# Kernel tuning notes

Hardware: AMD Instinct MI355X
Metric: run time of the kernel (lower is better)

Reference implementation:

```python
import jax, jax.numpy as jnp
import numpy as np

N_HEADS = 16
ROPE_BASE = 10000.0


def apply_rope(x):
    # x: [B, H, T, D]; rotate interleaved pairs along last dim, positions along T
    B, H, T, D = x.shape
    half = D // 2
    inv_freq = 1.0 / (ROPE_BASE ** (jnp.arange(0, half, dtype=jnp.float32) * 2.0 / D))
    angles = jnp.arange(T, dtype=jnp.float32)[:, None] * inv_freq[None, :]  # [T, half]
    cos = jnp.cos(angles).astype(x.dtype)  # [T, half]
    sin = jnp.sin(angles).astype(x.dtype)
    xp = x.reshape(B, H, T, half, 2)
    x1, x2 = xp[..., 0], xp[..., 1]
    out = jnp.stack([x1 * cos - x2 * sin, x1 * sin + x2 * cos], axis=-1)
    return out.reshape(B, H, T, D)


def setup_inputs() -> dict:
    key = jax.random.key(0)
    k1, k2, k3 = jax.random.split(key, 3)
    C = 1024
    x = jax.random.normal(k1, (2, 2048, C), dtype=jnp.float32)
    w_qkv = jax.random.normal(k2, (C, 3 * C), dtype=jnp.float32) * (1.0 / np.sqrt(C))
    w_out = jax.random.normal(k3, (C, C), dtype=jnp.float32) * (1.0 / np.sqrt(C))
    return {"x": x, "w_qkv": w_qkv, "w_out": w_out}


def reference(x, w_qkv, w_out):
    B, T, C = x.shape
    H = N_HEADS
    D = C // H
    qkv = (x @ w_qkv).reshape(B, T, 3, H, D)
    q, k, v = qkv[:, :, 0], qkv[:, :, 1], qkv[:, :, 2]  # [B, T, H, D]
    q = jnp.transpose(q, (0, 2, 1, 3))  # [B, H, T, D]
    k = jnp.transpose(k, (0, 2, 1, 3))
    v = jnp.transpose(v, (0, 2, 1, 3))
    q = apply_rope(q)
    k = apply_rope(k)
    scale = 1.0 / np.sqrt(D)
    scores = jnp.einsum('bhqd,bhkd->bhqk', q, k) * scale
    causal = jnp.tril(jnp.ones((T, T), dtype=bool))
    scores = jnp.where(causal, scores, jnp.finfo(scores.dtype).min)
    attn = jax.nn.softmax(scores, axis=-1)
    out = jnp.einsum('bhqk,bhkd->bhqd', attn, v)  # [B, H, T, D]
    out = jnp.transpose(out, (0, 2, 1, 3)).reshape(B, T, C)
    return out @ w_out
```

## Files before the change

kernel.cpp:

```cpp
#include <hip/hip_runtime.h>
#include <hip/hip_bf16.h>

typedef __attribute__((ext_vector_type(8))) short v8s;
typedef __attribute__((ext_vector_type(4))) float v4f;
typedef __attribute__((ext_vector_type(16))) float v16f;

typedef const __attribute__((address_space(1))) void* gas_ptr;
typedef __attribute__((address_space(3))) void* las_ptr;

#define MFMA16(a, b, c) __builtin_amdgcn_mfma_f32_16x16x32_bf16((a), (b), (c), 0, 0, 0)
#define MFMA32(a, b, c) __builtin_amdgcn_mfma_f32_32x32x16_bf16((a), (b), (c), 0, 0, 0)

__device__ __forceinline__ void gload_lds16(const void* g, void* l) {
  __builtin_amdgcn_global_load_lds((gas_ptr)g, (las_ptr)l, 16, 0, 0);
}

__device__ __forceinline__ unsigned short f2bf(float f) {
  unsigned int u = __float_as_uint(f);
  u += 0x7FFFu + ((u >> 16) & 1u);
  return (unsigned short)(u >> 16);
}
__device__ __forceinline__ float bf2f(unsigned short h) {
  return __uint_as_float(((unsigned int)h) << 16);
}

__device__ __forceinline__ unsigned cvt_pk_bf16(float lo, float hi) {
  unsigned r;
  asm("v_cvt_pk_bf16_f32 %0, %1, %2" : "=v"(r) : "v"(lo), "v"(hi));
  return r;
}

__global__ __launch_bounds__(256) void k_convert(const float* __restrict__ in,
                                                 unsigned short* __restrict__ out, int n4) {
  int i = blockIdx.x * 256 + threadIdx.x;
  if (i >= n4) return;
  float4 v = ((const float4*)in)[i];
  ushort4 o;
  o.x = f2bf(v.x); o.y = f2bf(v.y); o.z = f2bf(v.z); o.w = f2bf(v.w);
  ((ushort4*)out)[i] = o;
}

__global__ __launch_bounds__(256) void k_transpose_convert(const float* __restrict__ in,
                                                           unsigned short* __restrict__ out,
                                                           int R, int C) {
  __shared__ __attribute__((aligned(16))) unsigned short tb[64 * 72];
  const int r0 = blockIdx.y * 64, c0 = blockIdx.x * 64;
  const int tid = threadIdx.x;
#pragma unroll
  for (int j = 0; j < 4; ++j) {
    int slot = tid + 256 * j;
    int row = slot >> 4, q4 = (slot & 15) * 4;
    float4 v = *(const float4*)&in[(size_t)(r0 + row) * C + c0 + q4];
    ushort4 o;
    o.x = f2bf(v.x); o.y = f2bf(v.y); o.z = f2bf(v.z); o.w = f2bf(v.w);
    *(ushort4*)&tb[row * 72 + q4] = o;
  }
  __syncthreads();
#pragma unroll
  for (int j = 0; j < 4; ++j) {
    int slot = tid + 256 * j;
    int crow = slot >> 4, t4 = (slot & 15) * 4;
    ushort4 o;
    o.x = tb[(t4 + 0) * 72 + crow];
    o.y = tb[(t4 + 1) * 72 + crow];
    o.z = tb[(t4 + 2) * 72 + crow];
    o.w = tb[(t4 + 3) * 72 + crow];
    *(ushort4*)&out[(size_t)(c0 + crow) * R + r0 + t4] = o;
  }
}

template <bool F32OUT>
__global__ __launch_bounds__(256) void k_gemm(const unsigned short* __restrict__ A,
                                              const unsigned short* __restrict__ Bt,
                                              void* __restrict__ Cout,
                                              int M, int N, int K) {
  __shared__ __attribute__((aligned(16))) unsigned short As[128 * 32];
  __shared__ __attribute__((aligned(16))) unsigned short Bs[128 * 32];
  const int tid = threadIdx.x;
  const int w = tid >> 6, l = tid & 63, g = l >> 4, c = l & 15;
  const int wr = w >> 1, wc = w & 1;
  const int mt = blockIdx.y * 128, nt = blockIdx.x * 128;
  const int rowc = l >> 2, kslot = (l & 3) * 8;

  v4f acc[4][4];
#pragma unroll
  for (int m = 0; m < 4; ++m)
#pragma unroll
    for (int n = 0; n < 4; ++n) acc[m][n] = (v4f){0.f, 0.f, 0.f, 0.f};

  for (int kt = 0; kt < K; kt += 32) {
    __syncthreads();
#pragma unroll
    for (int i = 0; i < 2; ++i) {
      int ch = w + 4 * i;
      gload_lds16(&A[(size_t)(mt + ch * 16 + rowc) * K + kt + kslot], &As[ch * 512]);
      gload_lds16(&Bt[(size_t)(nt + ch * 16 + rowc) * K + kt + kslot], &Bs[ch * 512]);
    }
    __syncthreads();
    v8s af[4], bfr[4];
#pragma unroll
    for (int m = 0; m < 4; ++m)
      af[m] = *(const v8s*)&As[(wr * 64 + m * 16 + c) * 32 + g * 8];
#pragma unroll
    for (int n = 0; n < 4; ++n)
      bfr[n] = *(const v8s*)&Bs[(wc * 64 + n * 16 + c) * 32 + g * 8];
#pragma unroll
    for (int m = 0; m < 4; ++m)
#pragma unroll
      for (int n = 0; n < 4; ++n)
        acc[m][n] = MFMA16(af[m], bfr[n], acc[m][n]);
  }

#pragma unroll
  for (int m = 0; m < 4; ++m)
#pragma unroll
    for (int n = 0; n < 4; ++n)
#pragma unroll
      for (int r = 0; r < 4; ++r) {
        int row = mt + wr * 64 + m * 16 + g * 4 + r;
        int col = nt + wc * 64 + n * 16 + c;
        if (F32OUT)
          ((float*)Cout)[(size_t)row * N + col] = acc[m][n][r];
        else
          ((unsigned short*)Cout)[(size_t)row * N + col] = f2bf(acc[m][n][r]);
      }
}

__global__ __launch_bounds__(256) void k_post(const unsigned short* __restrict__ qkv,
                                              unsigned short* __restrict__ qp,
                                              unsigned short* __restrict__ kp,
                                              unsigned short* __restrict__ vp) {
  __shared__ float2 cs[64 * 32];
  __shared__ __attribute__((aligned(16))) unsigned short vt[64 * 72];
  const int bh = blockIdx.y;
  const int b = bh >> 4, hd = bh & 15;
  const int t0 = blockIdx.x * 64;
  const int tid = threadIdx.x;

#pragma unroll
  for (int e = 0; e < 8; ++e) {
    int idx = tid + 256 * e;
    int tl = idx >> 5, i = idx & 31;
    float invf = exp2f(-(float)i * 0.41524101186092034f);
    float ang = (float)(t0 + tl) * invf;
    float s, cc;
    sincosf(ang, &s, &cc);
    cs[idx] = make_float2(cc, s);
  }
#pragma unroll
  for (int j = 0; j < 2; ++j) {
    int slot = tid + 256 * j;
    int row = slot >> 3, c8 = (slot & 7) * 8;
    v8s vv = *(const v8s*)&qkv[(size_t)(b * 2048 + t0 + row) * 3072 + 2048 + hd * 64 + c8];
    *(v8s*)&vt[row * 72 + c8] = vv;
  }
  __syncthreads();

#pragma unroll
  for (int j = 0; j < 2; ++j) {
    int slot = tid + 256 * j;
    int row = slot >> 3, d0 = (slot & 7) * 8;
    int t = t0 + row;
    size_t base = (size_t)(b * 2048 + t) * 3072 + hd * 64;
    const int tile = t >> 5, c32 = t & 31, kd = d0 >> 4, hh = (d0 >> 3) & 1;
    const size_t pidx = (size_t)bh * 131072 + (tile * 4 + kd) * 512 + (hh * 32 + c32) * 8;
#pragma unroll
    for (int which = 0; which < 2; ++which) {
      const float qsc = which ? 1.0f : 0.18033688011112042f;
      v8s vq = *(const v8s*)&qkv[base + which * 1024 + d0];
      union { unsigned short s[8]; v8s v; } uo;
#pragma unroll
      for (int p = 0; p < 4; ++p) {
        float2 sc = cs[row * 32 + d0 / 2 + p];
        float x1 = bf2f((unsigned short)vq[2 * p]);
        float x2 = bf2f((unsigned short)vq[2 * p + 1]);
        uo.s[2 * p]     = f2bf((x1 * sc.x - x2 * sc.y) * qsc);
        uo.s[2 * p + 1] = f2bf((x1 * sc.y + x2 * sc.x) * qsc);
      }
      unsigned short* dst = which ? kp : qp;
      *(v8s*)&dst[pidx] = uo.v;
    }
  }

#pragma unroll
  for (int jj = 0; jj < 2; ++jj) {
    int idx = tid + 256 * jj;
    int tl = idx >> 8, kc = (idx >> 7) & 1, md = (idx >> 6) & 1;
    int lp = idx & 63, hh = lp >> 5, c32 = lp & 31;
    int d = md * 32 + c32;
    int brow = tl * 32 + kc * 16 + hh * 4;
    union { unsigned short s[8]; v8s v; } uo;
#pragma unroll
    for (int jh = 0; jh < 2; ++jh)
#pragma unroll
      for (int e = 0; e < 4; ++e)
        uo.s[jh * 4 + e] = vt[(brow + jh * 8 + e) * 72 + d];
    int tileG = (t0 >> 5) + tl;
    *(v8s*)&vp[(size_t)bh * 131072 + ((tileG * 2 + kc) * 2 + md) * 512 + lp * 8] = uo.v;
  }
}

__global__ __launch_bounds__(64) void k_attn(const unsigned short* __restrict__ qp,
                                             const unsigned short* __restrict__ kp,
                                             const unsigned short* __restrict__ vp,
                                             unsigned short* __restrict__ ao,
                                             char* __restrict__ part) {
  const int bid = (int)blockIdx.x;
  const int xcd = bid & 7, s2 = bid >> 3;
  const int bh = xcd + 8 * (s2 / 160);
  const int idx = 159 - (s2 % 160);
  int j, s;
  if (idx >= 96)      { j = 48 + ((idx - 96) >> 2); s = (idx - 96) & 3; }
  else if (idx >= 48) { j = 32 + (idx - 48) / 3;    s = (idx - 48) % 3; }
  else if (idx >= 16) { j = 16 + ((idx - 16) >> 1); s = (idx - 16) & 1; }
  else                { j = idx;                    s = 0; }
  const int t0 = s * 16;
  const int t1 = (t0 + 16 < j + 1) ? (t0 + 16) : (j + 1);

  const int l = threadIdx.x;
  const int c32 = l & 31, hh = l >> 5;
  const unsigned short* Qb = qp + (size_t)bh * 131072 + j * 4 * 512;
  const unsigned short* Kb = kp + (size_t)bh * 131072;
  const unsigned short* Vb = vp + (size_t)bh * 131072;

  v8s bq[4];
#pragma unroll
  for (int kd = 0; kd < 4; ++kd) bq[kd] = *(const v8s*)&Qb[kd * 512 + l * 8];

  v16f ot0 = {0,0,0,0,0,0,0,0,0,0,0,0,0,0,0,0};
  v16f ot1 = {0,0,0,0,0,0,0,0,0,0,0,0,0,0,0,0};
  float m2 = -1e30f, lsl = 0.f;

  v8s ak[4], av0[2][2], av1[2][2];
#pragma unroll
  for (int kd = 0; kd < 4; ++kd) ak[kd] = *(const v8s*)&Kb[(t0 * 4 + kd) * 512 + l * 8];
#pragma unroll
  for (int kc = 0; kc < 2; ++kc)
#pragma unroll
    for (int md = 0; md < 2; ++md)
      av0[kc][md] = *(const v8s*)&Vb[((t0 * 2 + kc) * 2 + md) * 512 + l * 8];

  auto TILE = [&](int t, v8s (&avc)[2][2], v8s (&avn)[2][2]) {
    v16f st = {0,0,0,0,0,0,0,0,0,0,0,0,0,0,0,0};
    __builtin_amdgcn_s_setprio(1);
#pragma unroll
    for (int kd = 0; kd < 4; ++kd) st = MFMA32(ak[kd], bq[kd], st);
    __builtin_amdgcn_s_setprio(0);

    if (t + 1 < t1) {
#pragma unroll
      for (int kd = 0; kd < 4; ++kd)
        ak[kd] = *(const v8s*)&Kb[((t + 1) * 4 + kd) * 512 + l * 8];
#pragma unroll
      for (int kc = 0; kc < 2; ++kc)
#pragma unroll
        for (int md = 0; md < 2; ++md)
          avn[kc][md] = *(const v8s*)&Vb[(((t + 1) * 2 + kc) * 2 + md) * 512 + l * 8];
    }

    if (t == j) {
#pragma unroll
      for (int r = 0; r < 16; ++r) {
        int rloc = (r & 3) + 8 * (r >> 2) + 4 * hh;
        st[r] = (rloc <= c32) ? st[r] : -1e30f;
      }
    }

    float a0 = fmaxf(st[0], st[1]),   a1 = fmaxf(st[2], st[3]);
    float a2 = fmaxf(st[4], st[5]),   a3 = fmaxf(st[6], st[7]);
    float a4 = fmaxf(st[8], st[9]),   a5 = fmaxf(st[10], st[11]);
    float a6 = fmaxf(st[12], st[13]), a7 = fmaxf(st[14], st[15]);
    float b0m = fmaxf(fmaxf(a0, a1), fmaxf(a2, a3));
    float b1m = fmaxf(fmaxf(a4, a5), fmaxf(a6, a7));
    float pm = fmaxf(b0m, b1m);
    if (!__all(pm <= m2 + 8.f)) {
      float pmw = fmaxf(pm, __shfl_xor(pm, 32));
      float mn = fmaxf(m2, pmw);
      float al = exp2f(m2 - mn);
      m2 = mn;
      lsl *= al;
      ot0 *= al;
      ot1 *= al;
    }

#pragma unroll
    for (int r = 0; r < 16; ++r) st[r] = exp2f(st[r] - m2);
    float e0 = st[0] + st[1],   e1 = st[2] + st[3];
    float e2 = st[4] + st[5],   e3 = st[6] + st[7];
    float e4 = st[8] + st[9],   e5 = st[10] + st[11];
    float e6 = st[12] + st[13], e7 = st[14] + st[15];
    float f0 = e0 + e1, f1 = e2 + e3, f2 = e4 + e5, f3 = e6 + e7;
    lsl += (f0 + f1) + (f2 + f3);

    unsigned wd[8];
#pragma unroll
    for (int i = 0; i < 8; ++i) wd[i] = cvt_pk_bf16(st[2 * i], st[2 * i + 1]);
    union { unsigned u[4]; v8s v; } pb0, pb1;
    pb0.u[0] = wd[0]; pb0.u[1] = wd[1]; pb0.u[2] = wd[2]; pb0.u[3] = wd[3];
    pb1.u[0] = wd[4]; pb1.u[1] = wd[5]; pb1.u[2] = wd[6]; pb1.u[3] = wd[7];

    __builtin_amdgcn_s_setprio(1);
    ot0 = MFMA32(avc[0][0], pb0.v, ot0);
    ot1 = MFMA32(avc[0][1], pb0.v, ot1);
    ot0 = MFMA32(avc[1][0], pb1.v, ot0);
    ot1 = MFMA32(avc[1][1], pb1.v, ot1);
    __builtin_amdgcn_s_setprio(0);
  };

  int t = t0;
  for (; t + 1 < t1; t += 2) {
    TILE(t,     av0, av1);
    TILE(t + 1, av1, av0);
  }
  if (t < t1) TILE(t, av0, av1);

  const float ls = lsl + __shfl_xor(lsl, 32);
  const float inv = 1.f / ls;
  if (j < 16) {
    const int b = bh >> 4, hd = bh & 15;
    const int tq = j * 32 + c32;
    unsigned short* aop = ao + (size_t)(b * 2048 + tq) * 1024 + hd * 64;
#pragma unroll
    for (int md = 0; md < 2; ++md)
#pragma unroll
      for (int q = 0; q < 4; ++q) {
        const v16f& o = md ? ot1 : ot0;
        unsigned w0 = cvt_pk_bf16(o[4 * q + 0] * inv, o[4 * q + 1] * inv);
        unsigned w1 = cvt_pk_bf16(o[4 * q + 2] * inv, o[4 * q + 3] * inv);
        int d = md * 32 + 8 * q + 4 * hh;
        *(uint2*)&aop[d] = make_uint2(w0, w1);
      }
  } else {
    char* slot = part + ((size_t)bh * 160 + idx) * 4352;
#pragma unroll
    for (int md = 0; md < 2; ++md)
#pragma unroll
      for (int i = 0; i < 8; ++i) {
        const v16f& o = md ? ot1 : ot0;
        union { _Float16 h[2]; unsigned u; } pk;
        pk.h[0] = (_Float16)(o[2 * i] * inv);
        pk.h[1] = (_Float16)(o[2 * i + 1] * inv);
        *(unsigned*)(slot + ((md * 8 + i) * 64 + l) * 4) = pk.u;
      }
    if (hh == 0) {
      *(float*)(slot + 4096 + c32 * 4) = m2;
      *(float*)(slot + 4224 + c32 * 4) = ls;
    }
  }
}

__global__ __launch_bounds__(64) void k_comb(const char* __restrict__ part,
                                             unsigned short* __restrict__ ao) {
  const int bh = blockIdx.y;
  const int j = 16 + (int)blockIdx.x;
  const int g = j >> 4;
  const int nch = g + 1;
  const int l = threadIdx.x, c32 = l & 31, hh = l >> 5;
  const int baseg = (g == 1) ? 16 : (g == 2) ? 48 : 96;
  const int ord0 = baseg + (j - 16 * g) * nch;
  const char* base = part + (size_t)bh * 160 * 4352;

  float ms[4], lsv[4], wsc[4];
  float mfin = -1e30f;
#pragma unroll
  for (int s = 0; s < 4; ++s) {
    if (s < nch) {
      const char* sl = base + (size_t)(ord0 + s) * 4352;
      ms[s] = *(const float*)(sl + 4096 + c32 * 4);
      lsv[s] = *(const float*)(sl + 4224 + c32 * 4);
      mfin = fmaxf(mfin, ms[s]);
    }
  }
  float lfin = 0.f;
#pragma unroll
  for (int s = 0; s < 4; ++s) {
    if (s < nch) {
      wsc[s] = lsv[s] * exp2f(ms[s] - mfin);
      lfin += wsc[s];
    }
  }
  const float inv = 1.f / lfin;
#pragma unroll
  for (int s = 0; s < 4; ++s)
    if (s < nch) wsc[s] *= inv;

  const int b = bh >> 4, hd = bh & 15;
  const int t = j * 32 + c32;
  unsigned short* aop = ao + (size_t)(b * 2048 + t) * 1024 + hd * 64;
#pragma unroll
  for (int md = 0; md < 2; ++md)
#pragma unroll
    for (int q4 = 0; q4 < 4; ++q4) {
      const int w0 = md * 8 + 2 * q4;
      float a0 = 0.f, a1 = 0.f, a2 = 0.f, a3 = 0.f;
#pragma unroll
      for (int s = 0; s < 4; ++s) {
        if (s < nch) {
          const char* sl = base + (size_t)(ord0 + s) * 4352;
          unsigned u0 = *(const unsigned*)(sl + ((w0 + 0) * 64 + l) * 4);
          unsigned u1 = *(const unsigned*)(sl + ((w0 + 1) * 64 + l) * 4);
          union { unsigned u; _Float16 h[2]; } p0, p1;
          p0.u = u0; p1.u = u1;
          a0 += (float)p0.h[0] * wsc[s];
          a1 += (float)p0.h[1] * wsc[s];
          a2 += (float)p1.h[0] * wsc[s];
          a3 += (float)p1.h[1] * wsc[s];
        }
      }
      unsigned o0 = cvt_pk_bf16(a0, a1);
      unsigned o1 = cvt_pk_bf16(a2, a3);
      int d = md * 32 + 8 * q4 + 4 * hh;
      *(uint2*)&aop[d] = make_uint2(o0, o1);
    }
}

extern "C" void kernel_launch(void* const* d_in, const int* in_sizes, int n_in,
                              void* d_out, int out_size, void* d_ws, size_t ws_size,
                              hipStream_t stream) {
  const float* x     = (const float*)d_in[0];
  const float* w_qkv = (const float*)d_in[1];
  const float* w_out = (const float*)d_in[2];
  float* out = (float*)d_out;

  char* ws = (char*)d_ws;
  unsigned short* xbf = (unsigned short*)(ws);
  unsigned short* wqT = (unsigned short*)(ws + 8388608);
  unsigned short* woT = (unsigned short*)(ws + 14680064);
  unsigned short* qkv = (unsigned short*)(ws + 16777216);
  unsigned short* qp  = (unsigned short*)(ws + 41943040);
  unsigned short* kp  = (unsigned short*)(ws + 50331648);
  unsigned short* vp  = (unsigned short*)(ws + 58720256);
  char* part = (char*)(ws + 16777216);

  k_convert<<<4096, 256, 0, stream>>>(x, xbf, 1048576);
  k_transpose_convert<<<dim3(48, 16), 256, 0, stream>>>(w_qkv, wqT, 1024, 3072);
  k_transpose_convert<<<dim3(16, 16), 256, 0, stream>>>(w_out, woT, 1024, 1024);
  k_gemm<false><<<dim3(24, 32), 256, 0, stream>>>(xbf, wqT, qkv, 4096, 3072, 1024);
  k_post<<<dim3(32, 32), 256, 0, stream>>>(qkv, qp, kp, vp);
  k_attn<<<5120, 64, 0, stream>>>(qp, kp, vp, xbf , part);
  k_comb<<<dim3(48, 32), 64, 0, stream>>>(part, xbf);
  k_gemm<true><<<dim3(8, 32), 256, 0, stream>>>(xbf, woT, (void*)out, 4096, 1024, 1024);
}
```

Before: 149.2 us.

## Share K/V tiles across four query-tile waves via double-buffered LDS

```diff
diff --git a/kernel.cpp b/kernel.cpp
--- a/kernel.cpp
+++ b/kernel.cpp
@@ -200,24 +200,33 @@
   }
 }
 
-__global__ __launch_bounds__(64) void k_attn(const unsigned short* __restrict__ qp,
-                                             const unsigned short* __restrict__ kp,
-                                             const unsigned short* __restrict__ vp,
-                                             unsigned short* __restrict__ ao,
-                                             char* __restrict__ part) {
+__global__ __launch_bounds__(256) void k_attn(const unsigned short* __restrict__ qp,
+                                              const unsigned short* __restrict__ kp,
+                                              const unsigned short* __restrict__ vp,
+                                              unsigned short* __restrict__ ao,
+                                              char* __restrict__ part) {
+  __shared__ __attribute__((aligned(16))) unsigned short Ks[2][2048];
+  __shared__ __attribute__((aligned(16))) unsigned short Vs[2][2048];
+
+  const int bh = blockIdx.y;
+  const int wv = threadIdx.x >> 6;
   const int bid = (int)blockIdx.x;
-  const int xcd = bid & 7, s2 = bid >> 3;
-  const int bh = xcd + 8 * (s2 / 160);
-  const int idx = 159 - (s2 % 160);
-  int j, s;
-  if (idx >= 96)      { j = 48 + ((idx - 96) >> 2); s = (idx - 96) & 3; }
-  else if (idx >= 48) { j = 32 + (idx - 48) / 3;    s = (idx - 48) % 3; }
-  else if (idx >= 16) { j = 16 + ((idx - 16) >> 1); s = (idx - 16) & 1; }
-  else                { j = idx;                    s = 0; }
+  int s, q0;
+  if (bid < 16)      { s = 0; q0 = 15 - bid; }
+  else if (bid < 28) { s = 1; q0 = 11 - (bid - 16); }
+  else if (bid < 36) { s = 2; q0 = 7  - (bid - 28); }
+  else               { s = 3; q0 = 3  - (bid - 36); }
+  const int j = 16 * s + 4 * q0 + wv;
+  const int g = j >> 4;
+  const int baseg = (g == 0) ? 0 : (g == 1) ? 16 : (g == 2) ? 48 : 96;
+  const int idx = baseg + (j - 16 * g) * (g + 1) + s;
+
   const int t0 = s * 16;
-  const int t1 = (t0 + 16 < j + 1) ? (t0 + 16) : (j + 1);
-
-  const int l = threadIdx.x;
+  const int t1w = (t0 + 16 < j + 1) ? (t0 + 16) : (j + 1);
+  const int jmax = 16 * s + 4 * q0 + 3;
+  const int t1m = (t0 + 16 < jmax + 1) ? (t0 + 16) : (jmax + 1);
+
+  const int l = threadIdx.x & 63;
   const int c32 = l & 31, hh = l >> 5;
   const unsigned short* Qb = qp + (size_t)bh * 131072 + j * 4 * 512;
   const unsigned short* Kb = kp + (size_t)bh * 131072;
@@ -231,88 +240,84 @@
   v16f ot1 = {0,0,0,0,0,0,0,0,0,0,0,0,0,0,0,0};
   float m2 = -1e30f, lsl = 0.f;
 
-  v8s ak[4], av0[2][2], av1[2][2];
-#pragma unroll
-  for (int kd = 0; kd < 4; ++kd) ak[kd] = *(const v8s*)&Kb[(t0 * 4 + kd) * 512 + l * 8];
-#pragma unroll
-  for (int kc = 0; kc < 2; ++kc)
-#pragma unroll
-    for (int md = 0; md < 2; ++md)
-      av0[kc][md] = *(const v8s*)&Vb[((t0 * 2 + kc) * 2 + md) * 512 + l * 8];
-
-  auto TILE = [&](int t, v8s (&avc)[2][2], v8s (&avn)[2][2]) {
-    v16f st = {0,0,0,0,0,0,0,0,0,0,0,0,0,0,0,0};
-    __builtin_amdgcn_s_setprio(1);
-#pragma unroll
-    for (int kd = 0; kd < 4; ++kd) st = MFMA32(ak[kd], bq[kd], st);
-    __builtin_amdgcn_s_setprio(0);
-
-    if (t + 1 < t1) {
-#pragma unroll
-      for (int kd = 0; kd < 4; ++kd)
-        ak[kd] = *(const v8s*)&Kb[((t + 1) * 4 + kd) * 512 + l * 8];
+  gload_lds16(&Kb[((size_t)t0 * 4 + wv) * 512 + l * 8], &Ks[0][wv * 512]);
+  gload_lds16(&Vb[((size_t)t0 * 4 + wv) * 512 + l * 8], &Vs[0][wv * 512]);
+  __syncthreads();
+
+  for (int t = t0; t < t1m; ++t) {
+    const int buf = (t - t0) & 1;
+    if (t + 1 < t1m) {
+      gload_lds16(&Kb[((size_t)(t + 1) * 4 + wv) * 512 + l * 8], &Ks[buf ^ 1][wv * 512]);
+      gload_lds16(&Vb[((size_t)(t + 1) * 4 + wv) * 512 + l * 8], &Vs[buf ^ 1][wv * 512]);
+    }
+
+    if (t < t1w) {
+      v8s ak[4], av[2][2];
+#pragma unroll
+      for (int kd = 0; kd < 4; ++kd) ak[kd] = *(const v8s*)&Ks[buf][kd * 512 + l * 8];
 #pragma unroll
       for (int kc = 0; kc < 2; ++kc)
 #pragma unroll
         for (int md = 0; md < 2; ++md)
-          avn[kc][md] = *(const v8s*)&Vb[(((t + 1) * 2 + kc) * 2 + md) * 512 + l * 8];
-    }
-
-    if (t == j) {
-#pragma unroll
-      for (int r = 0; r < 16; ++r) {
-        int rloc = (r & 3) + 8 * (r >> 2) + 4 * hh;
-        st[r] = (rloc <= c32) ? st[r] : -1e30f;
-      }
-    }
-
-    float a0 = fmaxf(st[0], st[1]),   a1 = fmaxf(st[2], st[3]);
-    float a2 = fmaxf(st[4], st[5]),   a3 = fmaxf(st[6], st[7]);
-    float a4 = fmaxf(st[8], st[9]),   a5 = fmaxf(st[10], st[11]);
-    float a6 = fmaxf(st[12], st[13]), a7 = fmaxf(st[14], st[15]);
-    float b0m = fmaxf(fmaxf(a0, a1), fmaxf(a2, a3));
-    float b1m = fmaxf(fmaxf(a4, a5), fmaxf(a6, a7));
-    float pm = fmaxf(b0m, b1m);
-    if (!__all(pm <= m2 + 8.f)) {
-      float pmw = fmaxf(pm, __shfl_xor(pm, 32));
-      float mn = fmaxf(m2, pmw);
-      float al = exp2f(m2 - mn);
-      m2 = mn;
-      lsl *= al;
-      ot0 *= al;
-      ot1 *= al;
-    }
-
-#pragma unroll
-    for (int r = 0; r < 16; ++r) st[r] = exp2f(st[r] - m2);
-    float e0 = st[0] + st[1],   e1 = st[2] + st[3];
-    float e2 = st[4] + st[5],   e3 = st[6] + st[7];
-    float e4 = st[8] + st[9],   e5 = st[10] + st[11];
-    float e6 = st[12] + st[13], e7 = st[14] + st[15];
-    float f0 = e0 + e1, f1 = e2 + e3, f2 = e4 + e5, f3 = e6 + e7;
-    lsl += (f0 + f1) + (f2 + f3);
-
-    unsigned wd[8];
-#pragma unroll
-    for (int i = 0; i < 8; ++i) wd[i] = cvt_pk_bf16(st[2 * i], st[2 * i + 1]);
-    union { unsigned u[4]; v8s v; } pb0, pb1;
-    pb0.u[0] = wd[0]; pb0.u[1] = wd[1]; pb0.u[2] = wd[2]; pb0.u[3] = wd[3];
-    pb1.u[0] = wd[4]; pb1.u[1] = wd[5]; pb1.u[2] = wd[6]; pb1.u[3] = wd[7];
-
-    __builtin_amdgcn_s_setprio(1);
-    ot0 = MFMA32(avc[0][0], pb0.v, ot0);
-    ot1 = MFMA32(avc[0][1], pb0.v, ot1);
-    ot0 = MFMA32(avc[1][0], pb1.v, ot0);
-    ot1 = MFMA32(avc[1][1], pb1.v, ot1);
-    __builtin_amdgcn_s_setprio(0);
-  };
-
-  int t = t0;
-  for (; t + 1 < t1; t += 2) {
-    TILE(t,     av0, av1);
-    TILE(t + 1, av1, av0);
-  }
-  if (t < t1) TILE(t, av0, av1);
+          av[kc][md] = *(const v8s*)&Vs[buf][(kc * 2 + md) * 512 + l * 8];
+
+      v16f st = {0,0,0,0,0,0,0,0,0,0,0,0,0,0,0,0};
+      __builtin_amdgcn_s_setprio(1);
+#pragma unroll
+      for (int kd = 0; kd < 4; ++kd) st = MFMA32(ak[kd], bq[kd], st);
+      __builtin_amdgcn_s_setprio(0);
+
+      if (t == j) {
+#pragma unroll
+        for (int r = 0; r < 16; ++r) {
+          int rloc = (r & 3) + 8 * (r >> 2) + 4 * hh;
+          st[r] = (rloc <= c32) ? st[r] : -1e30f;
+        }
+      }
+
+      float a0 = fmaxf(st[0], st[1]),   a1 = fmaxf(st[2], st[3]);
+      float a2 = fmaxf(st[4], st[5]),   a3 = fmaxf(st[6], st[7]);
+      float a4 = fmaxf(st[8], st[9]),   a5 = fmaxf(st[10], st[11]);
+      float a6 = fmaxf(st[12], st[13]), a7 = fmaxf(st[14], st[15]);
+      float b0m = fmaxf(fmaxf(a0, a1), fmaxf(a2, a3));
+      float b1m = fmaxf(fmaxf(a4, a5), fmaxf(a6, a7));
+      float pm = fmaxf(b0m, b1m);
+      if (!__all(pm <= m2 + 8.f)) {
+        float pmw = fmaxf(pm, __shfl_xor(pm, 32));
+        float mn = fmaxf(m2, pmw);
+        float al = exp2f(m2 - mn);
+        m2 = mn;
+        lsl *= al;
+        ot0 *= al;
+        ot1 *= al;
+      }
+
+#pragma unroll
+      for (int r = 0; r < 16; ++r) st[r] = exp2f(st[r] - m2);
+      float e0 = st[0] + st[1],   e1 = st[2] + st[3];
+      float e2 = st[4] + st[5],   e3 = st[6] + st[7];
+      float e4 = st[8] + st[9],   e5 = st[10] + st[11];
+      float e6 = st[12] + st[13], e7 = st[14] + st[15];
+      float f0 = e0 + e1, f1 = e2 + e3, f2 = e4 + e5, f3 = e6 + e7;
+      lsl += (f0 + f1) + (f2 + f3);
+
+      unsigned wd[8];
+#pragma unroll
+      for (int i = 0; i < 8; ++i) wd[i] = cvt_pk_bf16(st[2 * i], st[2 * i + 1]);
+      union { unsigned u[4]; v8s v; } pb0, pb1;
+      pb0.u[0] = wd[0]; pb0.u[1] = wd[1]; pb0.u[2] = wd[2]; pb0.u[3] = wd[3];
+      pb1.u[0] = wd[4]; pb1.u[1] = wd[5]; pb1.u[2] = wd[6]; pb1.u[3] = wd[7];
+
+      __builtin_amdgcn_s_setprio(1);
+      ot0 = MFMA32(av[0][0], pb0.v, ot0);
+      ot1 = MFMA32(av[0][1], pb0.v, ot1);
+      ot0 = MFMA32(av[1][0], pb1.v, ot0);
+      ot1 = MFMA32(av[1][1], pb1.v, ot1);
+      __builtin_amdgcn_s_setprio(0);
+    }
+
+    __syncthreads();
+  }
 
   const float ls = lsl + __shfl_xor(lsl, 32);
   const float inv = 1.f / ls;
@@ -437,7 +442,7 @@
   k_transpose_convert<<<dim3(16, 16), 256, 0, stream>>>(w_out, woT, 1024, 1024);
   k_gemm<false><<<dim3(24, 32), 256, 0, stream>>>(xbf, wqT, qkv, 4096, 3072, 1024);
   k_post<<<dim3(32, 32), 256, 0, stream>>>(qkv, qp, kp, vp);
-  k_attn<<<5120, 64, 0, stream>>>(qp, kp, vp, xbf , part);
+  k_attn<<<dim3(40, 32), 256, 0, stream>>>(qp, kp, vp, xbf , part);
   k_comb<<<dim3(48, 32), 64, 0, stream>>>(part, xbf);
   k_gemm<true><<<dim3(8, 32), 256, 0, stream>>>(xbf, woT, (void*)out, 4096, 1024, 1024);
 }
```

Measured after the change: 155.5 us. 4.2% more time.

## Template GEMM tile width and remap workgroups across XCDs

Applied to the files above, without the earlier changes.

```diff
diff --git a/kernel.cpp b/kernel.cpp
--- a/kernel.cpp
+++ b/kernel.cpp
@@ -69,56 +69,68 @@
   }
 }
 
-template <bool F32OUT>
+template <bool F32OUT, int BN, int WAVES_M, int WAVES_N>
 __global__ __launch_bounds__(256) void k_gemm(const unsigned short* __restrict__ A,
                                               const unsigned short* __restrict__ Bt,
                                               void* __restrict__ Cout,
                                               int M, int N, int K) {
+  constexpr int WM = 128 / (WAVES_M * 16);
+  constexpr int WN = BN / (WAVES_N * 16);
   __shared__ __attribute__((aligned(16))) unsigned short As[128 * 32];
-  __shared__ __attribute__((aligned(16))) unsigned short Bs[128 * 32];
+  __shared__ __attribute__((aligned(16))) unsigned short Bs[BN * 32];
   const int tid = threadIdx.x;
   const int w = tid >> 6, l = tid & 63, g = l >> 4, c = l & 15;
-  const int wr = w >> 1, wc = w & 1;
-  const int mt = blockIdx.y * 128, nt = blockIdx.x * 128;
+  const int wr = w / WAVES_N, wc = w % WAVES_N;
+
+  const int nwg = gridDim.x * gridDim.y;
+  const int orig = blockIdx.y * gridDim.x + blockIdx.x;
+  const int wgid = (orig & 7) * (nwg >> 3) + (orig >> 3);
+  const int mt = (wgid / gridDim.x) * 128;
+  const int nt = (wgid % gridDim.x) * BN;
+
   const int rowc = l >> 2, kslot = (l & 3) * 8;
 
-  v4f acc[4][4];
-#pragma unroll
-  for (int m = 0; m < 4; ++m)
-#pragma unroll
-    for (int n = 0; n < 4; ++n) acc[m][n] = (v4f){0.f, 0.f, 0.f, 0.f};
-
+  v4f acc[WM][WN];
+#pragma unroll
+  for (int m = 0; m < WM; ++m)
+#pragma unroll
+    for (int n = 0; n < WN; ++n) acc[m][n] = (v4f){0.f, 0.f, 0.f, 0.f};
+
+  constexpr int NCHUNK = 8 + BN / 16;
   for (int kt = 0; kt < K; kt += 32) {
     __syncthreads();
 #pragma unroll
-    for (int i = 0; i < 2; ++i) {
-      int ch = w + 4 * i;
-      gload_lds16(&A[(size_t)(mt + ch * 16 + rowc) * K + kt + kslot], &As[ch * 512]);
-      gload_lds16(&Bt[(size_t)(nt + ch * 16 + rowc) * K + kt + kslot], &Bs[ch * 512]);
+    for (int ch = 0; ch < NCHUNK; ch += 4) {
+      int cc = ch + w;
+      if (cc < 8)
+        gload_lds16(&A[(size_t)(mt + cc * 16 + rowc) * K + kt + kslot], &As[cc * 512]);
+      else
+        gload_lds16(&Bt[(size_t)(nt + (cc - 8) * 16 + rowc) * K + kt + kslot],
+                    &Bs[(cc - 8) * 512]);
     }
     __syncthreads();
-    v8s af[4], bfr[4];
-#pragma unroll
-    for (int m = 0; m < 4; ++m)
-      af[m] = *(const v8s*)&As[(wr * 64 + m * 16 + c) * 32 + g * 8];
-#pragma unroll
-    for (int n = 0; n < 4; ++n)
-      bfr[n] = *(const v8s*)&Bs[(wc * 64 + n * 16 + c) * 32 + g * 8];
-#pragma unroll
-    for (int m = 0; m < 4; ++m)
-#pragma unroll
-      for (int n = 0; n < 4; ++n)
+    v8s af[WM], bfr[WN];
+#pragma unroll
+    for (int m = 0; m < WM; ++m)
+      af[m] = *(const v8s*)&As[(wr * (WM * 16) + m * 16 + c) * 32 + g * 8];
+#pragma unroll
+    for (int n = 0; n < WN; ++n)
+      bfr[n] = *(const v8s*)&Bs[(wc * (WN * 16) + n * 16 + c) * 32 + g * 8];
+#pragma unroll
+    for (int m = 0; m < WM; ++m)
+#pragma unroll
+      for (int n = 0; n < WN; ++n)
         acc[m][n] = MFMA16(af[m], bfr[n], acc[m][n]);
   }
 
 #pragma unroll
-  for (int m = 0; m < 4; ++m)
-#pragma unroll
-    for (int n = 0; n < 4; ++n)
+  for (int m = 0; m < WM; ++m)
+#pragma unroll
+    for (int n = 0; n < WN; ++n)
 #pragma unroll
       for (int r = 0; r < 4; ++r) {
-        int row = mt + wr * 64 + m * 16 + g * 4 + r;
-        int col = nt + wc * 64 + n * 16 + c;
+        int row = mt + wr * (WM * 16) + m * 16 + g * 4 + r;
+        int col = nt + wc * (WN * 16) + n * 16 + c;
         if (F32OUT)
           ((float*)Cout)[(size_t)row * N + col] = acc[m][n][r];
         else
@@ -435,9 +447,9 @@
   k_convert<<<4096, 256, 0, stream>>>(x, xbf, 1048576);
   k_transpose_convert<<<dim3(48, 16), 256, 0, stream>>>(w_qkv, wqT, 1024, 3072);
   k_transpose_convert<<<dim3(16, 16), 256, 0, stream>>>(w_out, woT, 1024, 1024);
-  k_gemm<false><<<dim3(24, 32), 256, 0, stream>>>(xbf, wqT, qkv, 4096, 3072, 1024);
+  k_gemm<false, 128, 2, 2><<<dim3(24, 32), 256, 0, stream>>>(xbf, wqT, qkv, 4096, 3072, 1024);
   k_post<<<dim3(32, 32), 256, 0, stream>>>(qkv, qp, kp, vp);
   k_attn<<<5120, 64, 0, stream>>>(qp, kp, vp, xbf , part);
   k_comb<<<dim3(48, 32), 64, 0, stream>>>(part, xbf);
-  k_gemm<true><<<dim3(8, 32), 256, 0, stream>>>(xbf, woT, (void*)out, 4096, 1024, 1024);
-}
+  k_gemm<true, 64, 4, 1><<<dim3(16, 32), 256, 0, stream>>>(xbf, woT, (void*)out, 4096, 1024, 1024);
+}
```

Measured after the change: 139.5 us. -6.5%, faster.
